# Optimization experiments

Hardware: AMD Instinct MI355X
Metric: run time of the kernel (lower is better)

The kernel has to match this reference:

```python
import jax, jax.numpy as jnp
import numpy as np

B, L, D = 4, 4096, 1024

def setup_inputs() -> dict:
    key = jax.random.key(0)
    k1, k2, k3 = jax.random.split(key, 3)
    limit = float(np.sqrt(6.0 / (D + D)))  # glorot_uniform
    return {
        "x": jax.random.normal(k1, (B, L, D), dtype=jnp.float32),
        "state": jnp.zeros((B, D), dtype=jnp.float32),
        "erase_kernel": jax.random.uniform(k2, (D, D), minval=-limit, maxval=limit, dtype=jnp.float32),
        "erase_bias": jnp.zeros((D,), dtype=jnp.float32),
        "write_kernel": jax.random.uniform(k3, (D, D), minval=-limit, maxval=limit, dtype=jnp.float32),
        "write_bias": jnp.zeros((D,), dtype=jnp.float32),
    }

def reference(x, state, erase_kernel, erase_bias, write_kernel, write_bias):
    x = x.astype(jnp.float32)
    # Gates: [B, L, D]
    erase = jax.nn.sigmoid(jnp.einsum('bld,de->ble', x, erase_kernel) + erase_bias)
    write = jax.nn.sigmoid(jnp.einsum('bld,de->ble', x, write_kernel) + write_bias)

    def step(s, inp):
        e_t, w_t, x_t = inp  # each [B, D]
        s = s * (1.0 - e_t) + w_t * x_t
        return s, s

    # scan over time axis
    _, outs = jax.lax.scan(
        step, state,
        (jnp.swapaxes(erase, 0, 1), jnp.swapaxes(write, 0, 1), jnp.swapaxes(x, 0, 1)),
    )  # outs: [L, B, D]
    return jnp.swapaxes(outs, 0, 1)  # [B, L, D]
```

## Files before the change

kernel.cpp:

```cpp
#include <hip/hip_runtime.h>
#include <stdint.h>

#define MB (1ull << 20)

typedef __attribute__((ext_vector_type(8))) short bf16x8;
typedef __attribute__((ext_vector_type(8))) unsigned short u16x8;
typedef __attribute__((ext_vector_type(4))) float f32x4;

static __device__ __forceinline__ unsigned short f2bf(float f) {
    unsigned u = __builtin_bit_cast(unsigned, f);
    u += 0x7fffu + ((u >> 16) & 1u);
    return (unsigned short)(u >> 16);
}
static __device__ __forceinline__ float bf2f(unsigned short h) {
    return __builtin_bit_cast(float, ((unsigned)h) << 16);
}

__global__ __launch_bounds__(256) void cvt_x_kernel(const float* __restrict__ x,
                                                    unsigned short* __restrict__ xb, int n8) {
    int i = blockIdx.x * blockDim.x + threadIdx.x;
    if (i >= n8) return;
    const float4* px = (const float4*)x + (size_t)i * 2;
    float4 a = px[0], b = px[1];
    u16x8 o;
    o[0] = f2bf(a.x); o[1] = f2bf(a.y); o[2] = f2bf(a.z); o[3] = f2bf(a.w);
    o[4] = f2bf(b.x); o[5] = f2bf(b.y); o[6] = f2bf(b.z); o[7] = f2bf(b.w);
    ((u16x8*)xb)[i] = o;
}

__global__ __launch_bounds__(256) void cvt_w_kernel(const float* __restrict__ ek,
                                                    const float* __restrict__ wk,
                                                    unsigned short* __restrict__ wt) {
    int t = blockIdx.x * blockDim.x + threadIdx.x;
    int n = t >> 7;
    int kb = (t & 127) * 8;
    const float* src = (n < 1024) ? ek : wk;
    int col = n & 1023;
    u16x8 o;
#pragma unroll
    for (int j = 0; j < 8; ++j) o[j] = f2bf(src[(size_t)(kb + j) * 1024 + col]);
    ((u16x8*)wt)[t] = o;
}

template <bool HALFG>
__global__ __launch_bounds__(256) void gate_gemm(const unsigned short* __restrict__ Xb,
                                                 const unsigned short* __restrict__ Wt,
                                                 const float* __restrict__ eb,
                                                 const float* __restrict__ wb,
                                                 const float* __restrict__ xf,
                                                 void* __restrict__ AgV, void* __restrict__ WXgV) {
    __shared__ alignas(16) unsigned short As[128 * 32];
    __shared__ alignas(16) unsigned short Bs[128 * 32];
    const int tid = threadIdx.x;
    const int lane = tid & 63;
    const int w = tid >> 6;
    const int wr = w >> 1, wc = w & 1;
    const int m0 = blockIdx.x * 128;
    const int n0 = blockIdx.y * 128;
    const int colq = lane & 15, rowq = lane >> 4;

    const int smi = tid >> 2;
    const int skk = (tid & 3) * 8;

    f32x4 acc[4][4] = {};

    for (int k0 = 0; k0 < 1024; k0 += 32) {
        const unsigned short* sA0 = Xb + (size_t)(m0 + smi) * 1024 + k0 + skk;
        const unsigned short* sA1 = Xb + (size_t)(m0 + 64 + smi) * 1024 + k0 + skk;
        const unsigned short* sB0 = Wt + (size_t)(n0 + smi) * 1024 + k0 + skk;
        const unsigned short* sB1 = Wt + (size_t)(n0 + 64 + smi) * 1024 + k0 + skk;
        __builtin_amdgcn_global_load_lds((const __attribute__((address_space(1))) void*)sA0,
                                         (__attribute__((address_space(3))) void*)&As[tid * 8], 16, 0, 0);
        __builtin_amdgcn_global_load_lds((const __attribute__((address_space(1))) void*)sA1,
                                         (__attribute__((address_space(3))) void*)&As[2048 + tid * 8], 16, 0, 0);
        __builtin_amdgcn_global_load_lds((const __attribute__((address_space(1))) void*)sB0,
                                         (__attribute__((address_space(3))) void*)&Bs[tid * 8], 16, 0, 0);
        __builtin_amdgcn_global_load_lds((const __attribute__((address_space(1))) void*)sB1,
                                         (__attribute__((address_space(3))) void*)&Bs[2048 + tid * 8], 16, 0, 0);
        asm volatile("s_waitcnt vmcnt(0)" ::: "memory");
        __syncthreads();

        bf16x8 af[4], bfr[4];
#pragma unroll
        for (int f = 0; f < 4; ++f)
            af[f] = *(const bf16x8*)&As[(wr * 64 + f * 16 + colq) * 32 + rowq * 8];
#pragma unroll
        for (int f = 0; f < 4; ++f)
            bfr[f] = *(const bf16x8*)&Bs[(wc * 64 + f * 16 + colq) * 32 + rowq * 8];
#pragma unroll
        for (int i2 = 0; i2 < 4; ++i2)
#pragma unroll
            for (int j2 = 0; j2 < 4; ++j2)
                acc[i2][j2] = __builtin_amdgcn_mfma_f32_16x16x32_bf16(af[i2], bfr[j2], acc[i2][j2], 0, 0, 0);
        __syncthreads();
    }

    const bool isE = (n0 < 1024);
    const float* bias = isE ? eb : wb;
    const int nb = isE ? n0 : (n0 - 1024);
    void* outp = isE ? AgV : WXgV;
#pragma unroll
    for (int i2 = 0; i2 < 4; ++i2) {
        const int gmb = m0 + wr * 64 + i2 * 16 + rowq * 4;
#pragma unroll
        for (int j2 = 0; j2 < 4; ++j2) {
            const int gn = nb + wc * 64 + j2 * 16 + colq;
            const float bv = bias[gn];
#pragma unroll
            for (int r = 0; r < 4; ++r) {
                const size_t oidx = (size_t)(gmb + r) * 1024 + gn;
                const float z = acc[i2][j2][r] + bv;
                float val;
                if (isE) {
                    val = 1.0f / (1.0f + __expf(z));
                } else {
                    val = (1.0f / (1.0f + __expf(-z))) * xf[oidx];
                }
                if constexpr (HALFG) ((unsigned short*)outp)[oidx] = f2bf(val);
                else                 ((float*)outp)[oidx] = val;
            }
        }
    }
}

template <bool H>
__global__ __launch_bounds__(256) void scan_phase1(const void* __restrict__ Ag,
                                                   const void* __restrict__ WXg,
                                                   float* __restrict__ Asum, float* __restrict__ Bsum) {
    const int c = blockIdx.x, b = blockIdx.y, dz = blockIdx.z;
    const int d = dz * 256 + threadIdx.x;
    size_t base = ((size_t)(b * 4096 + c * 64)) * 1024 + d;
    float ap = 1.0f, s = 0.0f;
#pragma unroll 8
    for (int i = 0; i < 64; ++i) {
        float a, wx;
        if constexpr (H) {
            a = bf2f(((const unsigned short*)Ag)[base]);
            wx = bf2f(((const unsigned short*)WXg)[base]);
        } else {
            a = ((const float*)Ag)[base];
            wx = ((const float*)WXg)[base];
        }
        s = fmaf(s, a, wx);
        ap *= a;
        base += 1024;
    }
    const size_t so = ((size_t)(b * 64 + c)) * 1024 + d;
    Asum[so] = ap;
    Bsum[so] = s;
}

__global__ __launch_bounds__(256) void scan_phase2(const float* __restrict__ st,
                                                   const float* __restrict__ Asum,
                                                   const float* __restrict__ Bsum,
                                                   float* __restrict__ Sin) {
    const int t = blockIdx.x * 256 + threadIdx.x;
    const int b = t >> 10, d = t & 1023;
    float s = st[t];
    size_t idx = (size_t)(b * 64) * 1024 + d;
#pragma unroll 8
    for (int c = 0; c < 64; ++c) {
        Sin[idx] = s;
        s = fmaf(s, Asum[idx], Bsum[idx]);
        idx += 1024;
    }
}

template <bool H>
__global__ __launch_bounds__(256) void scan_phase3(const void* __restrict__ Ag,
                                                   const void* __restrict__ WXg,
                                                   const float* __restrict__ Sin,
                                                   float* __restrict__ out) {
    const int c = blockIdx.x, b = blockIdx.y, dz = blockIdx.z;
    const int d = dz * 256 + threadIdx.x;
    size_t base = ((size_t)(b * 4096 + c * 64)) * 1024 + d;
    float s = Sin[((size_t)(b * 64 + c)) * 1024 + d];
#pragma unroll 4
    for (int i = 0; i < 64; ++i) {
        float a, wx;
        if constexpr (H) {
            a = bf2f(((const unsigned short*)Ag)[base]);
            wx = bf2f(((const unsigned short*)WXg)[base]);
        } else {
            a = ((const float*)Ag)[base];
            wx = ((const float*)WXg)[base];
        }
        s = fmaf(s, a, wx);
        out[base] = s;
        base += 1024;
    }
}

extern "C" void kernel_launch(void* const* d_in, const int* in_sizes, int n_in,
                              void* d_out, int out_size, void* d_ws, size_t ws_size,
                              hipStream_t stream) {
    const float* x  = (const float*)d_in[0];
    const float* st = (const float*)d_in[1];
    const float* ek = (const float*)d_in[2];
    const float* eb = (const float*)d_in[3];
    const float* wk = (const float*)d_in[4];
    const float* wb = (const float*)d_in[5];
    float* out = (float*)d_out;
    char* ws = (char*)d_ws;

    unsigned short* xb = (unsigned short*)ws;
    unsigned short* wt = (unsigned short*)(ws + 32 * MB);
    const bool halfg = ws_size < 167 * MB;
    char* p = ws + 36 * MB;
    const size_t gbytes = halfg ? 32 * MB : 64 * MB;
    void* Ag = (void*)p;
    void* WXg = (void*)(p + gbytes);
    float* Asum = (float*)(p + 2 * gbytes);
    float* Bsum = Asum + (size_t)4 * 64 * 1024;
    float* Sin  = Bsum + (size_t)4 * 64 * 1024;

    cvt_x_kernel<<<8192, 256, 0, stream>>>(x, xb, 2097152);
    cvt_w_kernel<<<1024, 256, 0, stream>>>(ek, wk, wt);

    dim3 ggrid(128, 16);
    dim3 sgrid(64, 4, 4);
    if (halfg) {
        gate_gemm<true><<<ggrid, 256, 0, stream>>>(xb, wt, eb, wb, x, Ag, WXg);
        scan_phase1<true><<<sgrid, 256, 0, stream>>>(Ag, WXg, Asum, Bsum);
        scan_phase2<<<16, 256, 0, stream>>>(st, Asum, Bsum, Sin);
        scan_phase3<true><<<sgrid, 256, 0, stream>>>(Ag, WXg, Sin, out);
    } else {
        gate_gemm<false><<<ggrid, 256, 0, stream>>>(xb, wt, eb, wb, x, Ag, WXg);
        scan_phase1<false><<<sgrid, 256, 0, stream>>>(Ag, WXg, Asum, Bsum);
        scan_phase2<<<16, 256, 0, stream>>>(st, Asum, Bsum, Sin);
        scan_phase3<false><<<sgrid, 256, 0, stream>>>(Ag, WXg, Sin, out);
    }
}
```

Baseline: 321.3 us.

## Rewrite gate GEMM with 256x256 tiles, 4-stage LDS pipeline, swizzle; pack scan loads

Replaces the 128x128 gate GEMM with a 512-thread 256x256 tile kernel that uses a 4-deep global_load_lds ring buffer with partial vmcnt waits, XOR-swizzled LDS layout, block-index swizzling for L2 reuse and s_setprio around MFMAs. The scan phases now read two bf16 gates per 32-bit load and write float2 outputs. The fp32 gate path is removed, so gates are always stored as bf16. This targets GEMM latency stalls and narrow scan memory accesses. The cost is higher LDS use (128KB per block) and register pressure.

```diff
diff --git a/kernel.cpp b/kernel.cpp
--- a/kernel.cpp
+++ b/kernel.cpp
@@ -12,9 +12,13 @@
     u += 0x7fffu + ((u >> 16) & 1u);
     return (unsigned short)(u >> 16);
 }
-static __device__ __forceinline__ float bf2f(unsigned short h) {
-    return __builtin_bit_cast(float, ((unsigned)h) << 16);
-}
+static __device__ __forceinline__ float bf2f(unsigned u16) {
+    return __builtin_bit_cast(float, u16 << 16);
+}
+
+#define GLDS(gp, lp) __builtin_amdgcn_global_load_lds(                                   \
+        (const __attribute__((address_space(1))) void*)(gp),                             \
+        (__attribute__((address_space(3))) void*)(lp), 16, 0, 0)
 
 __global__ __launch_bounds__(256) void cvt_x_kernel(const float* __restrict__ x,
                                                     unsigned short* __restrict__ xb, int n8) {
@@ -42,112 +46,120 @@
     ((u16x8*)wt)[t] = o;
 }
 
-template <bool HALFG>
-__global__ __launch_bounds__(256) void gate_gemm(const unsigned short* __restrict__ Xb,
-                                                 const unsigned short* __restrict__ Wt,
-                                                 const float* __restrict__ eb,
-                                                 const float* __restrict__ wb,
-                                                 const float* __restrict__ xf,
-                                                 void* __restrict__ AgV, void* __restrict__ WXgV) {
-    __shared__ alignas(16) unsigned short As[128 * 32];
-    __shared__ alignas(16) unsigned short Bs[128 * 32];
+__global__ __launch_bounds__(512, 2) void gate_gemm(const unsigned short* __restrict__ Xb,
+                                                    const unsigned short* __restrict__ Wt,
+                                                    const float* __restrict__ eb,
+                                                    const float* __restrict__ wb,
+                                                    const float* __restrict__ xf,
+                                                    unsigned short* __restrict__ Ag,
+                                                    unsigned short* __restrict__ WXg) {
+    __shared__ alignas(16) unsigned short As[4][256 * 32];
+    __shared__ alignas(16) unsigned short Bs[4][256 * 32];
     const int tid = threadIdx.x;
     const int lane = tid & 63;
     const int w = tid >> 6;
-    const int wr = w >> 1, wc = w & 1;
-    const int m0 = blockIdx.x * 128;
-    const int n0 = blockIdx.y * 128;
+    const int wm = w >> 2, wn = w & 3;
     const int colq = lane & 15, rowq = lane >> 4;
 
-    const int smi = tid >> 2;
-    const int skk = (tid & 3) * 8;
-
-    f32x4 acc[4][4] = {};
-
-    for (int k0 = 0; k0 < 1024; k0 += 32) {
-        const unsigned short* sA0 = Xb + (size_t)(m0 + smi) * 1024 + k0 + skk;
-        const unsigned short* sA1 = Xb + (size_t)(m0 + 64 + smi) * 1024 + k0 + skk;
-        const unsigned short* sB0 = Wt + (size_t)(n0 + smi) * 1024 + k0 + skk;
-        const unsigned short* sB1 = Wt + (size_t)(n0 + 64 + smi) * 1024 + k0 + skk;
-        __builtin_amdgcn_global_load_lds((const __attribute__((address_space(1))) void*)sA0,
-                                         (__attribute__((address_space(3))) void*)&As[tid * 8], 16, 0, 0);
-        __builtin_amdgcn_global_load_lds((const __attribute__((address_space(1))) void*)sA1,
-                                         (__attribute__((address_space(3))) void*)&As[2048 + tid * 8], 16, 0, 0);
-        __builtin_amdgcn_global_load_lds((const __attribute__((address_space(1))) void*)sB0,
-                                         (__attribute__((address_space(3))) void*)&Bs[tid * 8], 16, 0, 0);
-        __builtin_amdgcn_global_load_lds((const __attribute__((address_space(1))) void*)sB1,
-                                         (__attribute__((address_space(3))) void*)&Bs[2048 + tid * 8], 16, 0, 0);
-        asm volatile("s_waitcnt vmcnt(0)" ::: "memory");
-        __syncthreads();
-
-        bf16x8 af[4], bfr[4];
+    const int orig = blockIdx.y * 64 + blockIdx.x;
+    const int swz = (orig & 7) * 64 + (orig >> 3);
+    const int m0 = (swz & 63) * 256;
+    const int n0g = (swz >> 6) * 256;
+
+    const int srow = tid >> 2;
+    const int ksrc = (((tid & 3) ^ ((tid >> 3) & 3)) * 8);
+    const int aslot = ((rowq ^ ((colq >> 1) & 3)) * 8);
+
+    f32x4 acc[8][4] = {};
+
+    auto stage = [&](int ts) {
+        const int bi = ts & 3;
+        const int k0 = (ts < 32 ? ts : 31) * 32;
+        const unsigned short* sa = Xb + (size_t)(m0 + srow) * 1024 + k0 + ksrc;
+        const unsigned short* sb = Wt + (size_t)(n0g + srow) * 1024 + k0 + ksrc;
+        unsigned short* la = &As[bi][tid * 8];
+        unsigned short* lb = &Bs[bi][tid * 8];
+        GLDS(sa, la);
+        GLDS(sa + 128 * 1024, la + 4096);
+        GLDS(sb, lb);
+        GLDS(sb + 128 * 1024, lb + 4096);
+    };
+
+    stage(0); stage(1); stage(2);
+
+    for (int t = 0; t < 32; ++t) {
+        stage(t + 3);
+        asm volatile("s_waitcnt vmcnt(12)" ::: "memory");
+        __builtin_amdgcn_s_barrier();
+        asm volatile("" ::: "memory");
+
+        const int bi = t & 3;
+        bf16x8 af[8], bfr[4];
+#pragma unroll
+        for (int f = 0; f < 8; ++f)
+            af[f] = *(const bf16x8*)&As[bi][(wm * 128 + f * 16 + colq) * 32 + aslot];
 #pragma unroll
         for (int f = 0; f < 4; ++f)
-            af[f] = *(const bf16x8*)&As[(wr * 64 + f * 16 + colq) * 32 + rowq * 8];
-#pragma unroll
-        for (int f = 0; f < 4; ++f)
-            bfr[f] = *(const bf16x8*)&Bs[(wc * 64 + f * 16 + colq) * 32 + rowq * 8];
-#pragma unroll
-        for (int i2 = 0; i2 < 4; ++i2)
+            bfr[f] = *(const bf16x8*)&Bs[bi][(wn * 64 + f * 16 + colq) * 32 + aslot];
+
+        __builtin_amdgcn_s_setprio(1);
+#pragma unroll
+        for (int i2 = 0; i2 < 8; ++i2)
 #pragma unroll
             for (int j2 = 0; j2 < 4; ++j2)
                 acc[i2][j2] = __builtin_amdgcn_mfma_f32_16x16x32_bf16(af[i2], bfr[j2], acc[i2][j2], 0, 0, 0);
-        __syncthreads();
-    }
-
-    const bool isE = (n0 < 1024);
+        __builtin_amdgcn_s_setprio(0);
+        asm volatile("" ::: "memory");
+        __builtin_amdgcn_s_barrier();
+    }
+
+    const bool isE = (n0g < 1024);
     const float* bias = isE ? eb : wb;
-    const int nb = isE ? n0 : (n0 - 1024);
-    void* outp = isE ? AgV : WXgV;
-#pragma unroll
-    for (int i2 = 0; i2 < 4; ++i2) {
-        const int gmb = m0 + wr * 64 + i2 * 16 + rowq * 4;
-#pragma unroll
-        for (int j2 = 0; j2 < 4; ++j2) {
-            const int gn = nb + wc * 64 + j2 * 16 + colq;
-            const float bv = bias[gn];
+    const int nb = isE ? n0g : (n0g - 1024);
+    unsigned short* outp = isE ? Ag : WXg;
+#pragma unroll
+    for (int j2 = 0; j2 < 4; ++j2) {
+        const int gn = nb + wn * 64 + j2 * 16 + colq;
+        const float bv = bias[gn];
+#pragma unroll
+        for (int i2 = 0; i2 < 8; ++i2) {
+            const int gm = m0 + wm * 128 + i2 * 16 + rowq * 4;
 #pragma unroll
             for (int r = 0; r < 4; ++r) {
-                const size_t oidx = (size_t)(gmb + r) * 1024 + gn;
+                const size_t oidx = (size_t)(gm + r) * 1024 + gn;
                 const float z = acc[i2][j2][r] + bv;
                 float val;
-                if (isE) {
-                    val = 1.0f / (1.0f + __expf(z));
-                } else {
-                    val = (1.0f / (1.0f + __expf(-z))) * xf[oidx];
-                }
-                if constexpr (HALFG) ((unsigned short*)outp)[oidx] = f2bf(val);
-                else                 ((float*)outp)[oidx] = val;
+                if (isE) val = 1.0f / (1.0f + __expf(z));
+                else     val = (1.0f / (1.0f + __expf(-z))) * xf[oidx];
+                outp[oidx] = f2bf(val);
             }
         }
     }
 }
 
-template <bool H>
-__global__ __launch_bounds__(256) void scan_phase1(const void* __restrict__ Ag,
-                                                   const void* __restrict__ WXg,
+__global__ __launch_bounds__(256) void scan_phase1(const unsigned short* __restrict__ Ag,
+                                                   const unsigned short* __restrict__ WXg,
                                                    float* __restrict__ Asum, float* __restrict__ Bsum) {
     const int c = blockIdx.x, b = blockIdx.y, dz = blockIdx.z;
-    const int d = dz * 256 + threadIdx.x;
-    size_t base = ((size_t)(b * 4096 + c * 64)) * 1024 + d;
-    float ap = 1.0f, s = 0.0f;
+    const int d2 = dz * 256 + threadIdx.x;
+    size_t base = ((size_t)(b * 4096 + c * 64)) * 512 + d2;
+    const unsigned* A2 = (const unsigned*)Ag;
+    const unsigned* W2 = (const unsigned*)WXg;
+    float ap0 = 1.f, ap1 = 1.f, s0 = 0.f, s1 = 0.f;
 #pragma unroll 8
     for (int i = 0; i < 64; ++i) {
-        float a, wx;
-        if constexpr (H) {
-            a = bf2f(((const unsigned short*)Ag)[base]);
-            wx = bf2f(((const unsigned short*)WXg)[base]);
-        } else {
-            a = ((const float*)Ag)[base];
-            wx = ((const float*)WXg)[base];
-        }
-        s = fmaf(s, a, wx);
-        ap *= a;
-        base += 1024;
-    }
-    const size_t so = ((size_t)(b * 64 + c)) * 1024 + d;
-    Asum[so] = ap;
-    Bsum[so] = s;
+        unsigned ua = A2[base], uw = W2[base];
+        float a0 = bf2f(ua & 0xffffu), a1 = bf2f(ua >> 16);
+        float w0 = bf2f(uw & 0xffffu), w1 = bf2f(uw >> 16);
+        s0 = fmaf(s0, a0, w0);
+        s1 = fmaf(s1, a1, w1);
+        ap0 *= a0;
+        ap1 *= a1;
+        base += 512;
+    }
+    const size_t so = ((size_t)(b * 64 + c)) * 512 + d2;
+    ((float2*)Asum)[so] = make_float2(ap0, ap1);
+    ((float2*)Bsum)[so] = make_float2(s0, s1);
 }
 
 __global__ __launch_bounds__(256) void scan_phase2(const float* __restrict__ st,
@@ -166,28 +178,25 @@
     }
 }
 
-template <bool H>
-__global__ __launch_bounds__(256) void scan_phase3(const void* __restrict__ Ag,
-                                                   const void* __restrict__ WXg,
+__global__ __launch_bounds__(256) void scan_phase3(const unsigned short* __restrict__ Ag,
+                                                   const unsigned short* __restrict__ WXg,
                                                    const float* __restrict__ Sin,
                                                    float* __restrict__ out) {
     const int c = blockIdx.x, b = blockIdx.y, dz = blockIdx.z;
-    const int d = dz * 256 + threadIdx.x;
-    size_t base = ((size_t)(b * 4096 + c * 64)) * 1024 + d;
-    float s = Sin[((size_t)(b * 64 + c)) * 1024 + d];
+    const int d2 = dz * 256 + threadIdx.x;
+    size_t base = ((size_t)(b * 4096 + c * 64)) * 512 + d2;
+    const unsigned* A2 = (const unsigned*)Ag;
+    const unsigned* W2 = (const unsigned*)WXg;
+    float2 sv = ((const float2*)Sin)[((size_t)(b * 64 + c)) * 512 + d2];
+    float s0 = sv.x, s1 = sv.y;
+    float2* o2 = (float2*)out;
 #pragma unroll 4
     for (int i = 0; i < 64; ++i) {
-        float a, wx;
-        if constexpr (H) {
-            a = bf2f(((const unsigned short*)Ag)[base]);
-            wx = bf2f(((const unsigned short*)WXg)[base]);
-        } else {
-            a = ((const float*)Ag)[base];
-            wx = ((const float*)WXg)[base];
-        }
-        s = fmaf(s, a, wx);
-        out[base] = s;
-        base += 1024;
+        unsigned ua = A2[base], uw = W2[base];
+        s0 = fmaf(s0, bf2f(ua & 0xffffu), bf2f(uw & 0xffffu));
+        s1 = fmaf(s1, bf2f(ua >> 16), bf2f(uw >> 16));
+        o2[base] = make_float2(s0, s1);
+        base += 512;
     }
 }
 
@@ -205,29 +214,20 @@
 
     unsigned short* xb = (unsigned short*)ws;
     unsigned short* wt = (unsigned short*)(ws + 32 * MB);
-    const bool halfg = ws_size < 167 * MB;
-    char* p = ws + 36 * MB;
-    const size_t gbytes = halfg ? 32 * MB : 64 * MB;
-    void* Ag = (void*)p;
-    void* WXg = (void*)(p + gbytes);
-    float* Asum = (float*)(p + 2 * gbytes);
+    unsigned short* Ag = (unsigned short*)(ws + 36 * MB);
+    unsigned short* WXg = (unsigned short*)(ws + 68 * MB);
+    float* Asum = (float*)(ws + 100 * MB);
     float* Bsum = Asum + (size_t)4 * 64 * 1024;
     float* Sin  = Bsum + (size_t)4 * 64 * 1024;
 
     cvt_x_kernel<<<8192, 256, 0, stream>>>(x, xb, 2097152);
     cvt_w_kernel<<<1024, 256, 0, stream>>>(ek, wk, wt);
 
-    dim3 ggrid(128, 16);
-    dim3 sgrid(64, 4, 4);
-    if (halfg) {
-        gate_gemm<true><<<ggrid, 256, 0, stream>>>(xb, wt, eb, wb, x, Ag, WXg);
-        scan_phase1<true><<<sgrid, 256, 0, stream>>>(Ag, WXg, Asum, Bsum);
-        scan_phase2<<<16, 256, 0, stream>>>(st, Asum, Bsum, Sin);
-        scan_phase3<true><<<sgrid, 256, 0, stream>>>(Ag, WXg, Sin, out);
-    } else {
-        gate_gemm<false><<<ggrid, 256, 0, stream>>>(xb, wt, eb, wb, x, Ag, WXg);
-        scan_phase1<false><<<sgrid, 256, 0, stream>>>(Ag, WXg, Asum, Bsum);
-        scan_phase2<<<16, 256, 0, stream>>>(st, Asum, Bsum, Sin);
-        scan_phase3<false><<<sgrid, 256, 0, stream>>>(Ag, WXg, Sin, out);
-    }
-}
+    dim3 ggrid(64, 8);
+    gate_gemm<<<ggrid, 512, 0, stream>>>(xb, wt, eb, wb, x, Ag, WXg);
+
+    dim3 sgrid(64, 4, 2);
+    scan_phase1<<<sgrid, 256, 0, stream>>>(Ag, WXg, Asum, Bsum);
+    scan_phase2<<<16, 256, 0, stream>>>(st, Asum, Bsum, Sin);
+    scan_phase3<<<sgrid, 256, 0, stream>>>(Ag, WXg, Sin, out);
+}
```

Measured after the change: 351.4 us. 1.09x slower.
